# Performance work log

Measured on AMD Instinct MI355X. Metric: run time of the kernel, lower is better.

The kernel has to match this reference:

```python
import jax, jax.numpy as jnp
import numpy as np

NUM_ITEMS = 100000
N = NUM_ITEMS + 1
D = 64
H = 2
DH = D // H
NB = 2
DFF = 256
MAXLEN = 50
GNN_LAYERS = 2
L_SHORT, L_LONG = 10, 50


def layernorm(x, g, b, eps=1e-5):
    m = jnp.mean(x, axis=-1, keepdims=True)
    v = jnp.var(x, axis=-1, keepdims=True)
    return (x - m) / jnp.sqrt(v + eps) * g + b


def setup_inputs() -> dict:
    key = jax.random.key(0)
    ks = jax.random.split(key, 16)
    B, S, E = 1024, MAXLEN, 1_000_000
    s = 0.05
    inp = {}
    inp['seq'] = jax.random.randint(ks[0], (B, S), 0, N)
    inp['lengths'] = jax.random.randint(ks[1], (B,), 1, S + 1)
    inp['edge_index'] = jax.random.randint(ks[2], (2, E), 0, N)
    inp['edge_weight'] = jax.random.uniform(ks[3], (E,), dtype=jnp.float32)
    inp['bert_emb'] = jax.random.normal(ks[4], (N, D), dtype=jnp.float32) * s
    inp['gnn_emb'] = jax.random.normal(ks[5], (N, D), dtype=jnp.float32) * s
    inp['gnn_proj_w'] = jax.random.normal(ks[6], (D, D), dtype=jnp.float32) * s
    inp['gnn_proj_b'] = jnp.zeros((D,), jnp.float32)
    inp['pos_emb'] = jax.random.normal(ks[7], (MAXLEN, D), dtype=jnp.float32) * s
    inp['wq'] = jax.random.normal(ks[8], (NB, D, D), dtype=jnp.float32) * s
    inp['wk'] = jax.random.normal(ks[9], (NB, D, D), dtype=jnp.float32) * s
    inp['wv'] = jax.random.normal(ks[10], (NB, D, D), dtype=jnp.float32) * s
    inp['wo'] = jax.random.normal(ks[11], (NB, D, D), dtype=jnp.float32) * s
    inp['w1'] = jax.random.normal(ks[12], (NB, D, DFF), dtype=jnp.float32) * s
    inp['b1'] = jnp.zeros((NB, DFF), jnp.float32)
    inp['w2'] = jax.random.normal(ks[13], (NB, DFF, D), dtype=jnp.float32) * s
    inp['b2'] = jnp.zeros((NB, D), jnp.float32)
    inp['ln1_g'] = jnp.ones((NB, D), jnp.float32)
    inp['ln1_b'] = jnp.zeros((NB, D), jnp.float32)
    inp['ln2_g'] = jnp.ones((NB, D), jnp.float32)
    inp['ln2_b'] = jnp.zeros((NB, D), jnp.float32)
    inp['lnf_g'] = jnp.ones((D,), jnp.float32)
    inp['lnf_b'] = jnp.zeros((D,), jnp.float32)
    return inp


def reference(seq, lengths, edge_index, edge_weight, bert_emb, gnn_emb,
              gnn_proj_w, gnn_proj_b, pos_emb, wq, wk, wv, wo,
              w1, b1, w2, b2, ln1_g, ln1_b, ln2_g, ln2_b, lnf_g, lnf_b):
    B, S = seq.shape
    src, dst = edge_index[0], edge_index[1]

    # --- LightGCN: weighted neighbor aggregation, mean over layer outputs ---
    x = gnn_emb
    acc = gnn_emb
    for _ in range(GNN_LAYERS):
        x = jax.ops.segment_sum(x[src] * edge_weight[:, None], dst, num_segments=N)
        acc = acc + x
    gnn_out = acc / (GNN_LAYERS + 1)
    gnn_out = gnn_out @ gnn_proj_w + gnn_proj_b  # gnn_projection

    # --- Discrete fusion: per-user alpha from sequence length ---
    alpha = jnp.where(lengths <= L_SHORT, 0.3,
                      jnp.where(lengths >= L_LONG, 0.7, 0.5)).astype(bert_emb.dtype)
    # Gather-then-blend: identical math to materializing the full
    # [B, N, D] fused table and gathering rows by seq indices.
    seq_emb = (alpha[:, None, None] * bert_emb[seq]
               + (1.0 - alpha)[:, None, None] * gnn_out[seq])  # [B,S,D]

    x = seq_emb + pos_emb[None, :S, :]
    key_mask = (seq != 0)  # [B,S] key-side padding mask

    scale = 1.0 / np.sqrt(DH).astype(np.float32)
    for i in range(NB):
        q = (x @ wq[i]).reshape(B, S, H, DH)
        k = (x @ wk[i]).reshape(B, S, H, DH)
        v = (x @ wv[i]).reshape(B, S, H, DH)
        scores = jnp.einsum('bqhd,bkhd->bhqk', q, k) * scale
        scores = jnp.where(key_mask[:, None, None, :], scores, -1e9)
        attn = jax.nn.softmax(scores, axis=-1)
        ctx = jnp.einsum('bhqk,bkhd->bqhd', attn, v).reshape(B, S, D)
        x = layernorm(x + ctx @ wo[i], ln1_g[i], ln1_b[i])
        h = jax.nn.gelu(x @ w1[i] + b1[i])
        x = layernorm(x + h @ w2[i] + b2[i], ln2_g[i], ln2_b[i])

    x = layernorm(x, lnf_g, lnf_b)
    seq_repr = x[jnp.arange(B), lengths - 1]  # [B, D]
    return seq_repr
```

## Files before the change

kernel.cpp:

```cpp
#include <hip/hip_runtime.h>
#include <math.h>


typedef __attribute__((ext_vector_type(8))) short bf16x8;
typedef __attribute__((ext_vector_type(4))) float f32x4;

#define SD   64
#define SS   50
#define NBLK 2
#define PH   72
#define OVCAP 8192

__device__ __forceinline__ short f2b(float f) {
  union { __bf16 h; short s; } u;
  u.h = (__bf16)f;
  return u.s;
}
__device__ __forceinline__ float b2f(short s) {
  union { unsigned u; float f; } v;
  v.u = ((unsigned)(unsigned short)s) << 16;
  return v.f;
}
__device__ __forceinline__ unsigned packb(float a, float b) {
  union { __bf16 h; unsigned short s; } ua, ub;
  ua.h = (__bf16)a; ub.h = (__bf16)b;
  return (unsigned)ua.s | ((unsigned)ub.s << 16);
}
__device__ __forceinline__ float2 wred_sum2(float a, float b) {
#pragma unroll
  for (int o = 32; o > 0; o >>= 1) {
    a += __shfl_xor(a, o, 64);
    b += __shfl_xor(b, o, 64);
  }
  return make_float2(a, b);
}
__device__ __forceinline__ float gelu_fast(float x) {
  float u = 0.7978845608028654f * x * (1.0f + 0.044715f * x * x);
  float e = __expf(-2.f * u);
  return x * __builtin_amdgcn_rcpf(1.0f + e);
}

__device__ __forceinline__ bf16x8 ldB(const short* __restrict__ Wb, int tile, int lane) {
  return *(const bf16x8*)(Wb + ((size_t)tile * 64 + lane) * 8);
}

__device__ __forceinline__ void mm64(const short* A, const short* __restrict__ Wb,
                                     int arow, int quad, int lane, f32x4 o4[4]) {
  bf16x8 a0 = *(const bf16x8*)(A + arow * PH + quad * 8);
  bf16x8 a1 = *(const bf16x8*)(A + arow * PH + 32 + quad * 8);
#pragma unroll
  for (int nt = 0; nt < 4; ++nt) {
    f32x4 acc = {0.f, 0.f, 0.f, 0.f};
    acc = __builtin_amdgcn_mfma_f32_16x16x32_bf16(a0, ldB(Wb, 0 * 4 + nt, lane), acc, 0, 0, 0);
    acc = __builtin_amdgcn_mfma_f32_16x16x32_bf16(a1, ldB(Wb, 1 * 4 + nt, lane), acc, 0, 0, 0);
    o4[nt] = acc;
  }
}

__device__ __forceinline__ void ln_epilogue(f32x4 o4[4], short* xh,
                                            const float* __restrict__ g,
                                            const float* __restrict__ bta,
                                            const float* __restrict__ extrab,
                                            int mt, int quad, int c0) {
  float vals[4][4];
  float s1[4] = {0.f, 0.f, 0.f, 0.f}, s2[4] = {0.f, 0.f, 0.f, 0.f};
#pragma unroll
  for (int nt = 0; nt < 4; ++nt) {
    int c = nt * 16 + c0;
    float eb = extrab ? extrab[c] : 0.f;
#pragma unroll
    for (int r = 0; r < 4; ++r) {
      int row = mt * 16 + quad * 4 + r;
      float v = o4[nt][r] + b2f(xh[row * PH + c]) + eb;
      vals[nt][r] = v;
      s1[r] += v;
      s2[r] += v * v;
    }
  }
#pragma unroll
  for (int o = 1; o < 16; o <<= 1) {
#pragma unroll
    for (int r = 0; r < 4; ++r) {
      s1[r] += __shfl_xor(s1[r], o, 64);
      s2[r] += __shfl_xor(s2[r], o, 64);
    }
  }
  float mv[4], rv[4];
#pragma unroll
  for (int r = 0; r < 4; ++r) {
    float m = s1[r] * (1.f / 64);
    float var = fmaxf(s2[r] * (1.f / 64) - m * m, 0.f);
    mv[r] = m;
    rv[r] = rsqrtf(var + 1e-5f);
  }
#pragma unroll
  for (int nt = 0; nt < 4; ++nt) {
    int c = nt * 16 + c0;
    float gv = g[c], bv = bta[c];
#pragma unroll
    for (int r = 0; r < 4; ++r) {
      int row = mt * 16 + quad * 4 + r;
      xh[row * PH + c] = f2b((vals[nt][r] - mv[r]) * rv[r] * gv + bv);
    }
  }
}

__device__ __forceinline__ void prep_body(int tid,
    const float* __restrict__ pw, const float* __restrict__ wq,
    const float* __restrict__ wk, const float* __restrict__ wv,
    const float* __restrict__ wo, const float* __restrict__ w1,
    const float* __restrict__ w2,
    short* __restrict__ pwB, short* __restrict__ wqB,
    short* __restrict__ wkB, short* __restrict__ wvB,
    short* __restrict__ woB, short* __restrict__ w1B,
    short* __restrict__ w2B) {
  int lane = tid & 63;
  int tile = tid >> 6;
  const float* W; short* out; int K, N, base;
  if (tile < 8)        { W = pw; out = pwB; K = 64;  N = 64;  base = 0; }
  else if (tile < 24)  { W = wq; out = wqB; K = 64;  N = 64;  base = 8; }
  else if (tile < 40)  { W = wk; out = wkB; K = 64;  N = 64;  base = 24; }
  else if (tile < 56)  { W = wv; out = wvB; K = 64;  N = 64;  base = 40; }
  else if (tile < 72)  { W = wo; out = woB; K = 64;  N = 64;  base = 56; }
  else if (tile < 136) { W = w1; out = w1B; K = 64;  N = 256; base = 72; }
  else if (tile < 200) { W = w2; out = w2B; K = 256; N = 64;  base = 136; }
  else return;
  int lt = tile - base;
  int KT = K / 32, NT = N / 16;
  int nt = lt % NT; lt /= NT;
  int kt = lt % KT; lt /= KT;
  int m = lt;
  const float* Wm = W + (size_t)m * K * N;
  int kbase = kt * 32 + ((lane >> 4) * 8);
  int n = nt * 16 + (lane & 15);
  short v[8];
#pragma unroll
  for (int j = 0; j < 8; ++j) v[j] = f2b(Wm[(size_t)(kbase + j) * N + n]);
  *(bf16x8*)(out + ((size_t)(tile - base) * 64 + lane) * 8) = *(bf16x8*)v;
}

__global__ void prep_zero(const float* __restrict__ pw, const float* __restrict__ wq,
                          const float* __restrict__ wk, const float* __restrict__ wv,
                          const float* __restrict__ wo, const float* __restrict__ w1,
                          const float* __restrict__ w2,
                          short* __restrict__ pwB, short* __restrict__ wqB,
                          short* __restrict__ wkB, short* __restrict__ wvB,
                          short* __restrict__ woB, short* __restrict__ w1B,
                          short* __restrict__ w2B,
                          const float* __restrict__ gnn, unsigned* __restrict__ gnnh,
                          int n32, int* __restrict__ cntp, int cntn,
                          int* __restrict__ flagsw, int nfw, int* __restrict__ ovcnt) {
  int tid = blockIdx.x * blockDim.x + threadIdx.x;
  int NT = gridDim.x * blockDim.x;
  prep_body(tid, pw, wq, wk, wv, wo, w1, w2, pwB, wqB, wkB, wvB, woB, w1B, w2B);
  for (int i = tid; i < cntn; i += NT) cntp[i] = 0;
  for (int i = tid; i < nfw; i += NT) flagsw[i] = 0;
  if (tid < 4) ovcnt[tid] = 0;
  for (int i = tid; i < n32; i += NT) {
    float2 f = ((const float2*)gnn)[i];
    gnnh[i] = packb(f.x, f.y);
  }
}

__global__ void gnn_build(const int* __restrict__ src, const int* __restrict__ dst,
                          const float* __restrict__ ew, int* __restrict__ cntp,
                          int cs, int cap, int2* __restrict__ ep,
                          int4* __restrict__ ov, int* __restrict__ ovcnt,
                          const int* __restrict__ seq,
                          unsigned char* __restrict__ flags, int BS,
                          int E, int Nn) {
  int tid = blockIdx.x * 256 + threadIdx.x;
  for (int i = tid; i < BS; i += gridDim.x * 256) flags[seq[i]] = 1;
  int p = blockIdx.x & 7;
  int sub = blockIdx.x >> 3;
  int nsub = gridDim.x >> 3;
  int lo = (int)(((long)p * Nn) >> 3);
  int hi = (int)(((long)(p + 1) * Nn) >> 3);
  for (int e = sub * 256 + threadIdx.x; e < E; e += nsub * 256) {
    int d = dst[e];
    if (d >= lo && d < hi) {
      int pos = atomicAdd(&cntp[d * cs], 1);
      if (pos < cap) {
        ep[(size_t)d * cap + pos] = make_int2(src[e], __float_as_int(ew[e]));
      } else {
        int oi = atomicAdd(ovcnt, 1);
        if (oi < OVCAP) ov[oi] = make_int4(d, src[e], __float_as_int(ew[e]), 0);
      }
    }
  }
}

__device__ __forceinline__ void gather_accum(float a[8], const unsigned* __restrict__ tab,
                                             int srcn, float w, int g) {
  uint4 p = *(const uint4*)(tab + (size_t)srcn * 32 + g * 4);
  a[0] += b2f((short)(p.x & 0xFFFF)) * w;
  a[1] += b2f((short)(p.x >> 16)) * w;
  a[2] += b2f((short)(p.y & 0xFFFF)) * w;
  a[3] += b2f((short)(p.y >> 16)) * w;
  a[4] += b2f((short)(p.z & 0xFFFF)) * w;
  a[5] += b2f((short)(p.z >> 16)) * w;
  a[6] += b2f((short)(p.w & 0xFFFF)) * w;
  a[7] += b2f((short)(p.w >> 16)) * w;
}

__device__ __forceinline__ void gather_core(float a[8], int n, int slot, int g,
    const unsigned* __restrict__ tab, const int* __restrict__ cntp, int cs, int cap,
    const int2* __restrict__ ep, const int4* __restrict__ ov,
    const int* __restrict__ ovcnt) {
  int deg = cntp[n * cs];
  int end = min(deg, cap);
  for (int i = slot; i < end; i += 8) {
    int2 ee = ep[(size_t)n * cap + i];
    gather_accum(a, tab, ee.x, __int_as_float(ee.y), g);
  }
  if (deg > cap && slot == 0) {
    int ovn = min(*ovcnt, OVCAP);
    for (int i = 0; i < ovn; ++i) {
      int4 e = ov[i];
      if (e.x == n) gather_accum(a, tab, e.y, __int_as_float(e.z), g);
    }
  }
}

__global__ void gnn_gather1(const unsigned* __restrict__ xinh,
                            const int* __restrict__ cntp, int cs, int cap,
                            const int2* __restrict__ ep, const int4* __restrict__ ov,
                            const int* __restrict__ ovcnt,
                            unsigned* __restrict__ xouth, int Nn) {
  int n = blockIdx.x * 4 + (threadIdx.x >> 6);
  if (n >= Nn) return;
  int lane = threadIdx.x & 63;
  int slot = lane >> 3, g = lane & 7;
  float a[8] = {0.f, 0.f, 0.f, 0.f, 0.f, 0.f, 0.f, 0.f};
  gather_core(a, n, slot, g, xinh, cntp, cs, cap, ep, ov, ovcnt);
#pragma unroll
  for (int o = 8; o < 64; o <<= 1)
#pragma unroll
    for (int j = 0; j < 8; ++j) a[j] += __shfl_xor(a[j], o, 64);
  if (slot == 0) {
    uint4 o4;
    o4.x = packb(a[0], a[1]);
    o4.y = packb(a[2], a[3]);
    o4.z = packb(a[4], a[5]);
    o4.w = packb(a[6], a[7]);
    *(uint4*)(xouth + (size_t)n * 32 + g * 4) = o4;
  }
}

__global__ void gnn_gather_avg(const unsigned* __restrict__ x1h,
                               const int* __restrict__ cntp, int cs, int cap,
                               const int2* __restrict__ ep, const int4* __restrict__ ov,
                               const int* __restrict__ ovcnt,
                               const float* __restrict__ gnn,
                               unsigned* __restrict__ avgh, int Nn,
                               const unsigned char* __restrict__ flags) {
  int n = blockIdx.x * 4 + (threadIdx.x >> 6);
  if (n >= Nn) return;
  if (!flags[n]) return;
  int lane = threadIdx.x & 63;
  int slot = lane >> 3, g = lane & 7;
  float a[8] = {0.f, 0.f, 0.f, 0.f, 0.f, 0.f, 0.f, 0.f};
  gather_core(a, n, slot, g, x1h, cntp, cs, cap, ep, ov, ovcnt);
#pragma unroll
  for (int o = 8; o < 64; o <<= 1)
#pragma unroll
    for (int j = 0; j < 8; ++j) a[j] += __shfl_xor(a[j], o, 64);
  if (slot == 0) {
    uint4 own = *(const uint4*)(x1h + (size_t)n * 32 + g * 4);
    float4 g0 = *(const float4*)(gnn + (size_t)n * 64 + g * 8);
    float4 g1 = *(const float4*)(gnn + (size_t)n * 64 + g * 8 + 4);
    float v0 = (g0.x + b2f((short)(own.x & 0xFFFF)) + a[0]) * (1.f / 3.f);
    float v1 = (g0.y + b2f((short)(own.x >> 16)) + a[1]) * (1.f / 3.f);
    float v2 = (g0.z + b2f((short)(own.y & 0xFFFF)) + a[2]) * (1.f / 3.f);
    float v3 = (g0.w + b2f((short)(own.y >> 16)) + a[3]) * (1.f / 3.f);
    float v4 = (g1.x + b2f((short)(own.z & 0xFFFF)) + a[4]) * (1.f / 3.f);
    float v5 = (g1.y + b2f((short)(own.z >> 16)) + a[5]) * (1.f / 3.f);
    float v6 = (g1.z + b2f((short)(own.w & 0xFFFF)) + a[6]) * (1.f / 3.f);
    float v7 = (g1.w + b2f((short)(own.w >> 16)) + a[7]) * (1.f / 3.f);
    uint4 o4;
    o4.x = packb(v0, v1);
    o4.y = packb(v2, v3);
    o4.z = packb(v4, v5);
    o4.w = packb(v6, v7);
    *(uint4*)(avgh + (size_t)n * 32 + g * 4) = o4;
  }
}

__global__ void gnn_scatter(const float* __restrict__ xin,
                            const int* __restrict__ src,
                            const int* __restrict__ dst,
                            const float* __restrict__ ew,
                            float* __restrict__ xout, int E) {
  int gid = blockIdx.x * blockDim.x + threadIdx.x;
  int e = gid >> 6;
  int d = gid & 63;
  if (e >= E) return;
  atomicAdd(&xout[(size_t)dst[e] * SD + d], xin[(size_t)src[e] * SD + d] * ew[e]);
}
__global__ void avg_from_f32(const float* __restrict__ gnn, const float* __restrict__ g1,
                             const float* __restrict__ g2, unsigned* __restrict__ avgh,
                             int n32) {
  int i = blockIdx.x * blockDim.x + threadIdx.x;
  if (i >= n32) return;
  float2 a = ((const float2*)gnn)[i];
  float2 b = ((const float2*)g1)[i];
  float2 c = ((const float2*)g2)[i];
  avgh[i] = packb((a.x + b.x + c.x) * (1.f / 3.f), (a.y + b.y + c.y) * (1.f / 3.f));
}

__global__ __launch_bounds__(256, 3)
void seq_transformer(const int* __restrict__ seq, const int* __restrict__ lengths,
                     const float* __restrict__ bert, const short* __restrict__ avgh,
                     const float* __restrict__ pbias, const float* __restrict__ pos,
                     const short* __restrict__ pwB, const short* __restrict__ wqB,
                     const short* __restrict__ wkB, const short* __restrict__ wvB,
                     const short* __restrict__ woB, const short* __restrict__ w1B,
                     const short* __restrict__ w2B,
                     const float* __restrict__ b1, const float* __restrict__ b2,
                     const float* __restrict__ ln1g, const float* __restrict__ ln1b,
                     const float* __restrict__ ln2g, const float* __restrict__ ln2b,
                     const float* __restrict__ lnfg, const float* __restrict__ lnfb,
                     float* __restrict__ out) {
  __shared__ short xh[64 * PH];
  __shared__ short qh[64 * PH];
  __shared__ short kh[64 * PH];
  __shared__ short vt[64 * PH];
  __shared__ short s0[64 * PH];
  __shared__ int   sidx[64];

  const int t = threadIdx.x;
  const int lane = t & 63;
  const int mt = t >> 6;
  const int quad = lane >> 4;
  const int c0 = lane & 15;
  const int b = blockIdx.x;
  const int arow = mt * 16 + c0;

  if (t < 64) sidx[t] = (t < SS) ? seq[b * SS + t] : 0;
  __syncthreads();

  const int len = lengths[b];
  const float alpha = (len <= 10) ? 0.3f : ((len >= 50) ? 0.7f : 0.5f);
  const float isq = 0.17677669529663687f;

  float kbias[4];
#pragma unroll
  for (int nt = 0; nt < 4; ++nt) {
    int key = nt * 16 + c0;
    kbias[nt] = (key < SS && sidx[key] != 0) ? 0.f : -1e9f;
  }

#pragma unroll
  for (int ir = 0; ir < 16; ++ir) {
    int s = mt * 16 + ir;
    short v = 0;
    if (s < SS) v = avgh[(size_t)sidx[s] * SD + lane];
    qh[s * PH + lane] = v;
  }

  {
    f32x4 o4[4];
    mm64(qh, pwB, arow, quad, lane, o4);
#pragma unroll
    for (int nt = 0; nt < 4; ++nt) {
      int c = nt * 16 + c0;
      float pbv = pbias[c];
#pragma unroll
      for (int r = 0; r < 4; ++r) {
        int row = mt * 16 + quad * 4 + r;
        short ov = 0;
        if (row < SS) {
          float g = o4[nt][r] + pbv;
          float xv = alpha * bert[(size_t)sidx[row] * SD + c] +
                     (1.f - alpha) * g + pos[row * SD + c];
          ov = f2b(xv);
        }
        xh[row * PH + c] = ov;
      }
    }
  }

#pragma unroll 1
  for (int blk = 0; blk < NBLK; ++blk) {
    const short* Wq = wqB + blk * 4096;
    const short* Wk = wkB + blk * 4096;
    const short* Wv = wvB + blk * 4096;
    const short* Wo = woB + blk * 4096;
    const short* W1 = w1B + blk * 16384;
    const short* W2 = w2B + blk * 16384;

    __syncthreads();

    {
      f32x4 o4[4];
      mm64(xh, Wq, arow, quad, lane, o4);
#pragma unroll
      for (int nt = 0; nt < 4; ++nt) {
        int c = nt * 16 + c0;
#pragma unroll
        for (int r = 0; r < 4; ++r) qh[(mt * 16 + quad * 4 + r) * PH + c] = f2b(o4[nt][r]);
      }
      mm64(xh, Wk, arow, quad, lane, o4);
#pragma unroll
      for (int nt = 0; nt < 4; ++nt) {
        int c = nt * 16 + c0;
#pragma unroll
        for (int r = 0; r < 4; ++r) kh[(mt * 16 + quad * 4 + r) * PH + c] = f2b(o4[nt][r]);
      }
      mm64(xh, Wv, arow, quad, lane, o4);
#pragma unroll
      for (int nt = 0; nt < 4; ++nt) {
        int dim = nt * 16 + c0;
        unsigned p0 = packb(o4[nt][0], o4[nt][1]);
        unsigned p1 = packb(o4[nt][2], o4[nt][3]);
        *(uint2*)(vt + (size_t)dim * PH + mt * 16 + quad * 4) = make_uint2(p0, p1);
      }
    }
    __syncthreads();

#pragma unroll
    for (int h = 0; h < 2; ++h) {
      {
        bf16x8 aq = *(const bf16x8*)(qh + arow * PH + h * 32 + quad * 8);
        float p[4][4];
        float mx[4], sm[4];
#pragma unroll
        for (int nt = 0; nt < 4; ++nt) {
          int key = nt * 16 + c0;
          bf16x8 bk = *(const bf16x8*)(kh + key * PH + h * 32 + quad * 8);
          f32x4 acc = {0.f, 0.f, 0.f, 0.f};
          acc = __builtin_amdgcn_mfma_f32_16x16x32_bf16(aq, bk, acc, 0, 0, 0);
#pragma unroll
          for (int r = 0; r < 4; ++r) p[nt][r] = fmaf(acc[r], isq, kbias[nt]);
        }
#pragma unroll
        for (int r = 0; r < 4; ++r)
          mx[r] = fmaxf(fmaxf(p[0][r], p[1][r]), fmaxf(p[2][r], p[3][r]));
#pragma unroll
        for (int o = 1; o < 16; o <<= 1)
#pragma unroll
          for (int r = 0; r < 4; ++r) mx[r] = fmaxf(mx[r], __shfl_xor(mx[r], o, 64));
#pragma unroll
        for (int r = 0; r < 4; ++r) sm[r] = 0.f;
#pragma unroll
        for (int nt = 0; nt < 4; ++nt)
#pragma unroll
          for (int r = 0; r < 4; ++r) {
            float e = __expf(p[nt][r] - mx[r]);
            p[nt][r] = e;
            sm[r] += e;
          }
#pragma unroll
        for (int o = 1; o < 16; o <<= 1)
#pragma unroll
          for (int r = 0; r < 4; ++r) sm[r] += __shfl_xor(sm[r], o, 64);
#pragma unroll
        for (int r = 0; r < 4; ++r) {
          float inv = __builtin_amdgcn_rcpf(sm[r]);
          int q = mt * 16 + quad * 4 + r;
#pragma unroll
          for (int nt = 0; nt < 4; ++nt)
            s0[q * PH + nt * 16 + c0] = f2b(p[nt][r] * inv);
        }
      }
      {
        bf16x8 a0 = *(const bf16x8*)(s0 + arow * PH + quad * 8);
        bf16x8 a1 = *(const bf16x8*)(s0 + arow * PH + 32 + quad * 8);
#pragma unroll
        for (int nt = 0; nt < 2; ++nt) {
          int dim = h * 32 + nt * 16 + c0;
          bf16x8 b0 = *(const bf16x8*)(vt + (size_t)dim * PH + quad * 8);
          bf16x8 b1v = *(const bf16x8*)(vt + (size_t)dim * PH + 32 + quad * 8);
          f32x4 acc = {0.f, 0.f, 0.f, 0.f};
          acc = __builtin_amdgcn_mfma_f32_16x16x32_bf16(a0, b0, acc, 0, 0, 0);
          acc = __builtin_amdgcn_mfma_f32_16x16x32_bf16(a1, b1v, acc, 0, 0, 0);
#pragma unroll
          for (int r = 0; r < 4; ++r)
            qh[(mt * 16 + quad * 4 + r) * PH + dim] = f2b(acc[r]);
        }
      }
    }

    {
      f32x4 o4[4];
      mm64(qh, Wo, arow, quad, lane, o4);
      ln_epilogue(o4, xh, ln1g + blk * SD, ln1b + blk * SD, nullptr, mt, quad, c0);
    }

    f32x4 facc[4];
#pragma unroll
    for (int nt = 0; nt < 4; ++nt) facc[nt] = (f32x4){0.f, 0.f, 0.f, 0.f};
#pragma unroll 1
    for (int c = 0; c < 4; ++c) {
      {
        bf16x8 a0 = *(const bf16x8*)(xh + arow * PH + quad * 8);
        bf16x8 a1 = *(const bf16x8*)(xh + arow * PH + 32 + quad * 8);
#pragma unroll
        for (int nt = 0; nt < 4; ++nt) {
          int ntg = c * 4 + nt;
          f32x4 acc = {0.f, 0.f, 0.f, 0.f};
          acc = __builtin_amdgcn_mfma_f32_16x16x32_bf16(a0, ldB(W1, 0 * 16 + ntg, lane), acc, 0, 0, 0);
          acc = __builtin_amdgcn_mfma_f32_16x16x32_bf16(a1, ldB(W1, 1 * 16 + ntg, lane), acc, 0, 0, 0);
          int cc = nt * 16 + c0;
          float b1v = b1[blk * 256 + c * 64 + cc];
#pragma unroll
          for (int r = 0; r < 4; ++r)
            qh[(mt * 16 + quad * 4 + r) * PH + cc] = f2b(gelu_fast(acc[r] + b1v));
        }
      }
      {
        bf16x8 a0 = *(const bf16x8*)(qh + arow * PH + quad * 8);
        bf16x8 a1 = *(const bf16x8*)(qh + arow * PH + 32 + quad * 8);
#pragma unroll
        for (int nt = 0; nt < 4; ++nt) {
          facc[nt] = __builtin_amdgcn_mfma_f32_16x16x32_bf16(a0, ldB(W2, (2 * c) * 4 + nt, lane), facc[nt], 0, 0, 0);
          facc[nt] = __builtin_amdgcn_mfma_f32_16x16x32_bf16(a1, ldB(W2, (2 * c + 1) * 4 + nt, lane), facc[nt], 0, 0, 0);
        }
      }
    }

    ln_epilogue(facc, xh, ln2g + blk * SD, ln2b + blk * SD, b2 + blk * SD, mt, quad, c0);
  }
  __syncthreads();

  if (mt == 0) {
    int sl = len - 1;
    float val = b2f(xh[sl * PH + lane]);
    float2 ss = wred_sum2(val, val * val);
    float m = ss.x * (1.f / 64);
    float var = fmaxf(ss.y * (1.f / 64) - m * m, 0.f);
    float rs = rsqrtf(var + 1e-5f);
    out[b * SD + lane] = (val - m) * rs * lnfg[lane] + lnfb[lane];
  }
}

extern "C" void kernel_launch(void* const* d_in, const int* in_sizes, int n_in,
                              void* d_out, int out_size, void* d_ws, size_t ws_size,
                              hipStream_t stream) {
  const int*   seq   = (const int*)d_in[0];
  const int*   lens  = (const int*)d_in[1];
  const int*   ei    = (const int*)d_in[2];
  const float* ew    = (const float*)d_in[3];
  const float* bert  = (const float*)d_in[4];
  const float* gnn   = (const float*)d_in[5];
  const float* pw    = (const float*)d_in[6];
  const float* pb    = (const float*)d_in[7];
  const float* pos   = (const float*)d_in[8];
  const float* wq    = (const float*)d_in[9];
  const float* wk    = (const float*)d_in[10];
  const float* wv    = (const float*)d_in[11];
  const float* wo    = (const float*)d_in[12];
  const float* w1    = (const float*)d_in[13];
  const float* b1    = (const float*)d_in[14];
  const float* w2    = (const float*)d_in[15];
  const float* b2    = (const float*)d_in[16];
  const float* ln1g  = (const float*)d_in[17];
  const float* ln1b  = (const float*)d_in[18];
  const float* ln2g  = (const float*)d_in[19];
  const float* ln2b  = (const float*)d_in[20];
  const float* lnfg  = (const float*)d_in[21];
  const float* lnfb  = (const float*)d_in[22];
  float* out = (float*)d_out;

  const int E = in_sizes[2] / 2;
  const int B = in_sizes[0] / SS;
  const int N = in_sizes[4] / SD;
  const int BS = B * SS;

  const int* esrc = ei;
  const int* edst = ei + E;

  const int Nr = (N + 1023) & ~1023;
  const int NF = (N + 15) & ~15;
  const int n32 = N * 32;

  short* pwB; short* wqB; short* wkB; short* wvB; short* woB; short* w1B; short* w2B;
  unsigned* gnnh; unsigned* g1xh; unsigned* avgh;
  int* cntp; unsigned char* flags; int* ovcnt; int4* ov; int2* ep;
  int cs = 4, cap = 32;
  auto layout = [&](int cstride, int capv) -> size_t {
    pwB = (short*)d_ws;
    wqB = pwB + 4096;
    wkB = wqB + 8192;
    wvB = wkB + 8192;
    woB = wvB + 8192;
    w1B = woB + 8192;
    w2B = w1B + 32768;
    gnnh = (unsigned*)(w2B + 32768);
    g1xh = gnnh + (size_t)N * 32;
    cntp = (int*)(g1xh + (size_t)N * 32);
    flags = (unsigned char*)(cntp + (size_t)Nr * cstride);
    ovcnt = (int*)(flags + NF);
    ov = (int4*)(ovcnt + 4);
    ep = (int2*)(ov + OVCAP);
    avgh = gnnh;
    return (size_t)((char*)(ep + (size_t)N * capv) - (char*)d_ws);
  };
  size_t need = layout(4, 32); cs = 4; cap = 32;
  if (need > ws_size) { need = layout(1, 32); cs = 1; cap = 32; }
  if (need > ws_size) { need = layout(1, 24); cs = 1; cap = 24; }

  float* g1x = (float*)cntp;
  float* g2x = g1x + (size_t)N * SD;
  size_t need_fb = (size_t)((char*)(g2x + (size_t)N * SD) - (char*)d_ws);

  if (need <= ws_size) {
    const int cntn = Nr * cs;
    prep_zero<<<1024, 256, 0, stream>>>(pw, wq, wk, wv, wo, w1, w2,
                                        pwB, wqB, wkB, wvB, woB, w1B, w2B,
                                        gnn, gnnh, n32, cntp, cntn,
                                        (int*)flags, NF / 4, ovcnt);
    gnn_build<<<1024, 256, 0, stream>>>(esrc, edst, ew, cntp, cs, cap, ep,
                                        ov, ovcnt, seq, flags, BS, E, N);
    const int nb = (N + 3) / 4;
    gnn_gather1<<<nb, 256, 0, stream>>>(gnnh, cntp, cs, cap, ep, ov, ovcnt,
                                        g1xh, N);
    gnn_gather_avg<<<nb, 256, 0, stream>>>(g1xh, cntp, cs, cap, ep, ov, ovcnt,
                                           gnn, avgh, N, flags);
  } else if (ws_size >= need_fb) {
    prep_zero<<<1024, 256, 0, stream>>>(pw, wq, wk, wv, wo, w1, w2,
                                        pwB, wqB, wkB, wvB, woB, w1B, w2B,
                                        gnn, gnnh, n32, (int*)d_ws, 0,
                                        (int*)d_ws, 0, (int*)d_ws);
    hipMemsetAsync(g1x, 0, (size_t)2 * N * SD * sizeof(float), stream);
    const long total = (long)E * 64;
    const int sblocks = (int)((total + 255) / 256);
    gnn_scatter<<<sblocks, 256, 0, stream>>>(gnn, esrc, edst, ew, g1x, E);
    gnn_scatter<<<sblocks, 256, 0, stream>>>(g1x, esrc, edst, ew, g2x, E);
    avg_from_f32<<<(n32 + 255) / 256, 256, 0, stream>>>(gnn, g1x, g2x, avgh, n32);
  }

  seq_transformer<<<B, 256, 0, stream>>>(
      seq, lens, bert, (const short*)avgh, pb, pos,
      pwB, wqB, wkB, wvB, woB, w1B, w2B,
      b1, b2, ln1g, ln1b, ln2g, ln2b, lnfg, lnfb, out);
}
```

Baseline: 341.5 us.

## Fuse second LightGCN gather into transformer prologue, drop flags pass

The second-layer neighbor gather and averaging move into the seq_transformer prologue. Each block gathers only the rows it needs for its sequence, which removes the separate gnn_gather_avg kernel, the flag-marking pass and the flag zeroing. The trade-off is repeated gathers for items that occur in many sequences, plus extra latency-bound work inside the transformer kernel, which may hurt its occupancy. The fallback path is adapted so it produces layer sums for the in-kernel averaging.

```diff
diff --git a/kernel.cpp b/kernel.cpp
--- a/kernel.cpp
+++ b/kernel.cpp
@@ -149,12 +149,11 @@
                           short* __restrict__ w2B,
                           const float* __restrict__ gnn, unsigned* __restrict__ gnnh,
                           int n32, int* __restrict__ cntp, int cntn,
-                          int* __restrict__ flagsw, int nfw, int* __restrict__ ovcnt) {
+                          int* __restrict__ ovcnt) {
   int tid = blockIdx.x * blockDim.x + threadIdx.x;
   int NT = gridDim.x * blockDim.x;
   prep_body(tid, pw, wq, wk, wv, wo, w1, w2, pwB, wqB, wkB, wvB, woB, w1B, w2B);
   for (int i = tid; i < cntn; i += NT) cntp[i] = 0;
-  for (int i = tid; i < nfw; i += NT) flagsw[i] = 0;
   if (tid < 4) ovcnt[tid] = 0;
   for (int i = tid; i < n32; i += NT) {
     float2 f = ((const float2*)gnn)[i];
@@ -166,11 +165,7 @@
                           const float* __restrict__ ew, int* __restrict__ cntp,
                           int cs, int cap, int2* __restrict__ ep,
                           int4* __restrict__ ov, int* __restrict__ ovcnt,
-                          const int* __restrict__ seq,
-                          unsigned char* __restrict__ flags, int BS,
                           int E, int Nn) {
-  int tid = blockIdx.x * 256 + threadIdx.x;
-  for (int i = tid; i < BS; i += gridDim.x * 256) flags[seq[i]] = 1;
   int p = blockIdx.x & 7;
   int sub = blockIdx.x >> 3;
   int nsub = gridDim.x >> 3;
@@ -214,7 +209,7 @@
     gather_accum(a, tab, ee.x, __int_as_float(ee.y), g);
   }
   if (deg > cap && slot == 0) {
-    int ovn = min(*ovcnt, OVCAP);
+    int ovn = min(max(*ovcnt, 0), OVCAP);
     for (int i = 0; i < ovn; ++i) {
       int4 e = ov[i];
       if (e.x == n) gather_accum(a, tab, e.y, __int_as_float(e.z), g);
@@ -247,45 +242,22 @@
   }
 }
 
-__global__ void gnn_gather_avg(const unsigned* __restrict__ x1h,
-                               const int* __restrict__ cntp, int cs, int cap,
-                               const int2* __restrict__ ep, const int4* __restrict__ ov,
-                               const int* __restrict__ ovcnt,
-                               const float* __restrict__ gnn,
-                               unsigned* __restrict__ avgh, int Nn,
-                               const unsigned char* __restrict__ flags) {
-  int n = blockIdx.x * 4 + (threadIdx.x >> 6);
-  if (n >= Nn) return;
-  if (!flags[n]) return;
-  int lane = threadIdx.x & 63;
-  int slot = lane >> 3, g = lane & 7;
-  float a[8] = {0.f, 0.f, 0.f, 0.f, 0.f, 0.f, 0.f, 0.f};
-  gather_core(a, n, slot, g, x1h, cntp, cs, cap, ep, ov, ovcnt);
-#pragma unroll
-  for (int o = 8; o < 64; o <<= 1)
-#pragma unroll
-    for (int j = 0; j < 8; ++j) a[j] += __shfl_xor(a[j], o, 64);
-  if (slot == 0) {
-    uint4 own = *(const uint4*)(x1h + (size_t)n * 32 + g * 4);
-    float4 g0 = *(const float4*)(gnn + (size_t)n * 64 + g * 8);
-    float4 g1 = *(const float4*)(gnn + (size_t)n * 64 + g * 8 + 4);
-    float v0 = (g0.x + b2f((short)(own.x & 0xFFFF)) + a[0]) * (1.f / 3.f);
-    float v1 = (g0.y + b2f((short)(own.x >> 16)) + a[1]) * (1.f / 3.f);
-    float v2 = (g0.z + b2f((short)(own.y & 0xFFFF)) + a[2]) * (1.f / 3.f);
-    float v3 = (g0.w + b2f((short)(own.y >> 16)) + a[3]) * (1.f / 3.f);
-    float v4 = (g1.x + b2f((short)(own.z & 0xFFFF)) + a[4]) * (1.f / 3.f);
-    float v5 = (g1.y + b2f((short)(own.z >> 16)) + a[5]) * (1.f / 3.f);
-    float v6 = (g1.z + b2f((short)(own.w & 0xFFFF)) + a[6]) * (1.f / 3.f);
-    float v7 = (g1.w + b2f((short)(own.w >> 16)) + a[7]) * (1.f / 3.f);
-    uint4 o4;
-    o4.x = packb(v0, v1);
-    o4.y = packb(v2, v3);
-    o4.z = packb(v4, v5);
-    o4.w = packb(v6, v7);
-    *(uint4*)(avgh + (size_t)n * 32 + g * 4) = o4;
-  }
-}
-
+__global__ void prep_only(const float* __restrict__ pw, const float* __restrict__ wq,
+                          const float* __restrict__ wk, const float* __restrict__ wv,
+                          const float* __restrict__ wo, const float* __restrict__ w1,
+                          const float* __restrict__ w2,
+                          short* __restrict__ pwB, short* __restrict__ wqB,
+                          short* __restrict__ wkB, short* __restrict__ wvB,
+                          short* __restrict__ woB, short* __restrict__ w1B,
+                          short* __restrict__ w2B) {
+  prep_body(blockIdx.x * blockDim.x + threadIdx.x,
+            pw, wq, wk, wv, wo, w1, w2, pwB, wqB, wkB, wvB, woB, w1B, w2B);
+}
+__global__ void zero_ws(int* __restrict__ p, int n) {
+  int tid = blockIdx.x * blockDim.x + threadIdx.x;
+  int NT = gridDim.x * blockDim.x;
+  for (int i = tid; i < n; i += NT) p[i] = 0;
+}
 __global__ void gnn_scatter(const float* __restrict__ xin,
                             const int* __restrict__ src,
                             const int* __restrict__ dst,
@@ -297,20 +269,23 @@
   if (e >= E) return;
   atomicAdd(&xout[(size_t)dst[e] * SD + d], xin[(size_t)src[e] * SD + d] * ew[e]);
 }
-__global__ void avg_from_f32(const float* __restrict__ gnn, const float* __restrict__ g1,
-                             const float* __restrict__ g2, unsigned* __restrict__ avgh,
-                             int n32) {
+__global__ void sum2_to_bf16(const float* __restrict__ g1, const float* __restrict__ g2,
+                             unsigned* __restrict__ x1h, int n32) {
   int i = blockIdx.x * blockDim.x + threadIdx.x;
   if (i >= n32) return;
-  float2 a = ((const float2*)gnn)[i];
-  float2 b = ((const float2*)g1)[i];
-  float2 c = ((const float2*)g2)[i];
-  avgh[i] = packb((a.x + b.x + c.x) * (1.f / 3.f), (a.y + b.y + c.y) * (1.f / 3.f));
+  float2 a = ((const float2*)g1)[i];
+  float2 b = ((const float2*)g2)[i];
+  x1h[i] = packb(a.x + b.x, a.y + b.y);
 }
 
 __global__ __launch_bounds__(256, 3)
 void seq_transformer(const int* __restrict__ seq, const int* __restrict__ lengths,
-                     const float* __restrict__ bert, const short* __restrict__ avgh,
+                     const float* __restrict__ bert,
+                     const unsigned* __restrict__ x1h,
+                     const int* __restrict__ cntp, int cs, int cap,
+                     const int2* __restrict__ ep, const int4* __restrict__ ov,
+                     const int* __restrict__ ovcnt,
+                     const float* __restrict__ gnnf,
                      const float* __restrict__ pbias, const float* __restrict__ pos,
                      const short* __restrict__ pwB, const short* __restrict__ wqB,
                      const short* __restrict__ wkB, const short* __restrict__ wvB,
@@ -350,12 +325,36 @@
     kbias[nt] = (key < SS && sidx[key] != 0) ? 0.f : -1e9f;
   }
 
-#pragma unroll
-  for (int ir = 0; ir < 16; ++ir) {
-    int s = mt * 16 + ir;
-    short v = 0;
-    if (s < SS) v = avgh[(size_t)sidx[s] * SD + lane];
-    qh[s * PH + lane] = v;
+  {
+    const int slot = lane >> 3;
+    const int g8 = lane & 7;
+#pragma unroll 2
+    for (int ir = 0; ir < 16; ++ir) {
+      int s = mt * 16 + ir;
+      if (s >= SS) { qh[s * PH + lane] = 0; continue; }
+      int n = sidx[s];
+      float a[8] = {0.f, 0.f, 0.f, 0.f, 0.f, 0.f, 0.f, 0.f};
+      gather_core(a, n, slot, g8, x1h, cntp, cs, cap, ep, ov, ovcnt);
+#pragma unroll
+      for (int o = 8; o < 64; o <<= 1)
+#pragma unroll
+        for (int j = 0; j < 8; ++j) a[j] += __shfl_xor(a[j], o, 64);
+      if (slot == 0) {
+        uint4 own = *(const uint4*)(x1h + (size_t)n * 32 + g8 * 4);
+        float4 q0 = *(const float4*)(gnnf + (size_t)n * 64 + g8 * 8);
+        float4 q1 = *(const float4*)(gnnf + (size_t)n * 64 + g8 * 8 + 4);
+        short o8[8];
+        o8[0] = f2b((q0.x + b2f((short)(own.x & 0xFFFF)) + a[0]) * (1.f / 3.f));
+        o8[1] = f2b((q0.y + b2f((short)(own.x >> 16)) + a[1]) * (1.f / 3.f));
+        o8[2] = f2b((q0.z + b2f((short)(own.y & 0xFFFF)) + a[2]) * (1.f / 3.f));
+        o8[3] = f2b((q0.w + b2f((short)(own.y >> 16)) + a[3]) * (1.f / 3.f));
+        o8[4] = f2b((q1.x + b2f((short)(own.z & 0xFFFF)) + a[4]) * (1.f / 3.f));
+        o8[5] = f2b((q1.y + b2f((short)(own.z >> 16)) + a[5]) * (1.f / 3.f));
+        o8[6] = f2b((q1.z + b2f((short)(own.w & 0xFFFF)) + a[6]) * (1.f / 3.f));
+        o8[7] = f2b((q1.w + b2f((short)(own.w >> 16)) + a[7]) * (1.f / 3.f));
+        *(bf16x8*)(qh + s * PH + g8 * 8) = *(bf16x8*)o8;
+      }
+    }
   }
 
   {
@@ -368,14 +367,14 @@
 #pragma unroll
       for (int r = 0; r < 4; ++r) {
         int row = mt * 16 + quad * 4 + r;
-        short ov = 0;
+        short ov8 = 0;
         if (row < SS) {
           float g = o4[nt][r] + pbv;
           float xv = alpha * bert[(size_t)sidx[row] * SD + c] +
                      (1.f - alpha) * g + pos[row * SD + c];
-          ov = f2b(xv);
+          ov8 = f2b(xv);
         }
-        xh[row * PH + c] = ov;
+        xh[row * PH + c] = ov8;
       }
     }
   }
@@ -565,18 +564,16 @@
   const int E = in_sizes[2] / 2;
   const int B = in_sizes[0] / SS;
   const int N = in_sizes[4] / SD;
-  const int BS = B * SS;
 
   const int* esrc = ei;
   const int* edst = ei + E;
 
   const int Nr = (N + 1023) & ~1023;
-  const int NF = (N + 15) & ~15;
   const int n32 = N * 32;
 
   short* pwB; short* wqB; short* wkB; short* wvB; short* woB; short* w1B; short* w2B;
-  unsigned* gnnh; unsigned* g1xh; unsigned* avgh;
-  int* cntp; unsigned char* flags; int* ovcnt; int4* ov; int2* ep;
+  unsigned* gnnh; unsigned* g1xh;
+  int* cntp; int* ovcnt; int4* ov; int2* ep;
   int cs = 4, cap = 32;
   auto layout = [&](int cstride, int capv) -> size_t {
     pwB = (short*)d_ws;
@@ -589,18 +586,16 @@
     gnnh = (unsigned*)(w2B + 32768);
     g1xh = gnnh + (size_t)N * 32;
     cntp = (int*)(g1xh + (size_t)N * 32);
-    flags = (unsigned char*)(cntp + (size_t)Nr * cstride);
-    ovcnt = (int*)(flags + NF);
+    ovcnt = cntp + (size_t)Nr * cstride;
     ov = (int4*)(ovcnt + 4);
     ep = (int2*)(ov + OVCAP);
-    avgh = gnnh;
     return (size_t)((char*)(ep + (size_t)N * capv) - (char*)d_ws);
   };
   size_t need = layout(4, 32); cs = 4; cap = 32;
   if (need > ws_size) { need = layout(1, 32); cs = 1; cap = 32; }
   if (need > ws_size) { need = layout(1, 24); cs = 1; cap = 24; }
 
-  float* g1x = (float*)cntp;
+  float* g1x = (float*)ep;
   float* g2x = g1x + (size_t)N * SD;
   size_t need_fb = (size_t)((char*)(g2x + (size_t)N * SD) - (char*)d_ws);
 
@@ -608,30 +603,26 @@
     const int cntn = Nr * cs;
     prep_zero<<<1024, 256, 0, stream>>>(pw, wq, wk, wv, wo, w1, w2,
                                         pwB, wqB, wkB, wvB, woB, w1B, w2B,
-                                        gnn, gnnh, n32, cntp, cntn,
-                                        (int*)flags, NF / 4, ovcnt);
+                                        gnn, gnnh, n32, cntp, cntn, ovcnt);
     gnn_build<<<1024, 256, 0, stream>>>(esrc, edst, ew, cntp, cs, cap, ep,
-                                        ov, ovcnt, seq, flags, BS, E, N);
+                                        ov, ovcnt, E, N);
     const int nb = (N + 3) / 4;
     gnn_gather1<<<nb, 256, 0, stream>>>(gnnh, cntp, cs, cap, ep, ov, ovcnt,
                                         g1xh, N);
-    gnn_gather_avg<<<nb, 256, 0, stream>>>(g1xh, cntp, cs, cap, ep, ov, ovcnt,
-                                           gnn, avgh, N, flags);
   } else if (ws_size >= need_fb) {
-    prep_zero<<<1024, 256, 0, stream>>>(pw, wq, wk, wv, wo, w1, w2,
-                                        pwB, wqB, wkB, wvB, woB, w1B, w2B,
-                                        gnn, gnnh, n32, (int*)d_ws, 0,
-                                        (int*)d_ws, 0, (int*)d_ws);
-    hipMemsetAsync(g1x, 0, (size_t)2 * N * SD * sizeof(float), stream);
+    prep_only<<<50, 256, 0, stream>>>(pw, wq, wk, wv, wo, w1, w2,
+                                      pwB, wqB, wkB, wvB, woB, w1B, w2B);
+    zero_ws<<<1024, 256, 0, stream>>>(cntp, Nr * cs + 4);
+    zero_ws<<<1024, 256, 0, stream>>>((int*)g1x, 2 * N * SD);
     const long total = (long)E * 64;
     const int sblocks = (int)((total + 255) / 256);
     gnn_scatter<<<sblocks, 256, 0, stream>>>(gnn, esrc, edst, ew, g1x, E);
     gnn_scatter<<<sblocks, 256, 0, stream>>>(g1x, esrc, edst, ew, g2x, E);
-    avg_from_f32<<<(n32 + 255) / 256, 256, 0, stream>>>(gnn, g1x, g2x, avgh, n32);
+    sum2_to_bf16<<<(n32 + 255) / 256, 256, 0, stream>>>(g1x, g2x, g1xh, n32);
   }
 
   seq_transformer<<<B, 256, 0, stream>>>(
-      seq, lens, bert, (const short*)avgh, pb, pos,
+      seq, lens, bert, g1xh, cntp, cs, cap, ep, ov, ovcnt, gnn, pb, pos,
       pwB, wqB, wkB, wvB, woB, w1B, w2B,
       b1, b2, ln1g, ln1b, ln2g, ln2b, lnfg, lnfb, out);
 }
```

Measured after the change: 363.8 us. +6.5%, slower.
